# Performance work log

Hardware: AMD Instinct MI355X
Metric: run time of the kernel (lower is better)

The kernel has to match this reference:

```python
import jax, jax.numpy as jnp
import numpy as np

B, S, D = 2, 2048, 2048
H, HKV = 16, 4
HD = D // H  # 128
ROPE_BASE = 10000.0


def _rope(t, cos, sin):
    # t: [B, h, S, HD]; torch variant: x1 = even dims, x2 = odd dims,
    # output = concat([x1*cos - x2*sin, x1*sin + x2*cos], axis=-1)
    x1 = t[..., ::2]
    x2 = t[..., 1::2]
    return jnp.concatenate([x1 * cos - x2 * sin, x1 * sin + x2 * cos], axis=-1)


def setup_inputs() -> dict:
    key = jax.random.key(0)
    kx, kq, kk, kv, ko = jax.random.split(key, 5)
    x = jax.random.normal(kx, (B, S, D), dtype=jnp.float32)
    scale = 0.02
    Wq = jax.random.normal(kq, (D, H * HD), dtype=jnp.float32) * scale
    Wk = jax.random.normal(kk, (D, HKV * HD), dtype=jnp.float32) * scale
    Wv = jax.random.normal(kv, (D, HKV * HD), dtype=jnp.float32) * scale
    Wo = jax.random.normal(ko, (H * HD, D), dtype=jnp.float32) * scale
    mask = jnp.tril(jnp.ones((S, S), dtype=bool))  # causal
    return {"x": x, "Wq": Wq, "Wk": Wk, "Wv": Wv, "Wo": Wo, "mask": mask}


def reference(x, Wq, Wk, Wv, Wo, mask):
    b, s, d = x.shape
    # projections: [B,S,h,HD] -> [B,h,S,HD]
    q = (x @ Wq).reshape(b, s, H, HD).transpose(0, 2, 1, 3)
    k = (x @ Wk).reshape(b, s, HKV, HD).transpose(0, 2, 1, 3)
    v = (x @ Wv).reshape(b, s, HKV, HD).transpose(0, 2, 1, 3)

    # RoPE tables: [S, HD/2]
    theta = 1.0 / (ROPE_BASE ** (jnp.arange(0, HD, 2, dtype=jnp.float32) / HD))
    angles = jnp.arange(s, dtype=jnp.float32)[:, None] * theta
    cos, sin = jnp.cos(angles), jnp.sin(angles)

    q = _rope(q, cos, sin)
    k = _rope(k, cos, sin)

    # GQA: repeat_interleave kv heads along head dim
    rep = H // HKV
    k = jnp.repeat(k, rep, axis=1)
    v = jnp.repeat(v, rep, axis=1)

    scores = jnp.einsum("bhqd,bhkd->bhqk", q, k) / jnp.sqrt(jnp.float32(HD))
    scores = jnp.where(mask, scores, -jnp.inf)
    attn = jax.nn.softmax(scores, axis=-1)

    out = jnp.einsum("bhqk,bhkd->bqhd", attn, v).reshape(b, s, H * HD)
    return out @ Wo
```

## Files before the change

kernel.cpp:

```cpp
#include <hip/hip_runtime.h>

typedef __bf16 bf16;
typedef __bf16 bf16x8 __attribute__((ext_vector_type(8)));
typedef float f32x4 __attribute__((ext_vector_type(4)));
typedef short s16x4 __attribute__((ext_vector_type(4)));

#define B_ 2
#define S_ 2048
#define D_ 2048
#define H_ 16
#define HKV_ 4
#define HD_ 128
#define QKVW 3072
#define QKW 2560
#define SCALE 0.08838834764831845f
#define NEGINF -30000.0f

__device__ inline void gload16(const void* g, void* l) {
  __builtin_amdgcn_global_load_lds((const __attribute__((address_space(1))) unsigned int*)g,
                                   (__attribute__((address_space(3))) unsigned int*)l, 16, 0, 0);
}

__device__ inline unsigned short bfb(float v) {
  union { bf16 h; unsigned short u; } c;
  c.h = (bf16)v;
  return c.u;
}

__global__ void detect_dtype(const unsigned* __restrict__ xw, int* __restrict__ flag) {
  __shared__ int cnt;
  if (threadIdx.x == 0) cnt = 0;
  __syncthreads();
  unsigned w = xw[(size_t)threadIdx.x * 16384];
  unsigned low = w & 0xFFFFu;
  int e = (int)((low >> 7) & 0xFF);
  int vote = (low == 0u || (e >= 100 && e <= 140)) ? 1 : 0;
  atomicAdd(&cnt, vote);
  __syncthreads();
  if (threadIdx.x == 0) *flag = (cnt >= 128) ? 1 : 0;
}

__global__ __launch_bounds__(256) void transpose_qkvw(
    const void* __restrict__ Wq, const void* __restrict__ Wk, const void* __restrict__ Wv,
    bf16* __restrict__ wqkvT, const int* __restrict__ flag) {
  int z = blockIdx.z;
  const void* in = (z == 0) ? Wq : (z == 1) ? Wk : Wv;
  int cols = (z == 0) ? 2048 : 512;
  bf16* out = wqkvT + ((z == 0) ? 0 : (z == 1) ? 2048 * 2048 : 2560 * 2048);
  if (blockIdx.x * 32 >= cols) return;
  int fm = *flag;
  __shared__ float tile[32][33];
  int c0 = blockIdx.x * 32, r0 = blockIdx.y * 32;
  int tx = threadIdx.x, ty = threadIdx.y;
#pragma unroll
  for (int i = 0; i < 32; i += 8) {
    long idx = (long)(r0 + ty + i) * cols + c0 + tx;
    tile[ty + i][tx] = fm ? (float)((const bf16*)in)[idx] : ((const float*)in)[idx];
  }
  __syncthreads();
#pragma unroll
  for (int i = 0; i < 32; i += 8)
    out[(long)(c0 + ty + i) * 2048 + r0 + tx] = (bf16)tile[tx][ty + i];
}

__global__ __launch_bounds__(256) void transpose_cvt(
    const void* __restrict__ in, bf16* __restrict__ out,
    long in_stride, long out_stride, const int* __restrict__ flag) {
  __shared__ float tile[32][33];
  int fm = *flag;
  int c0 = blockIdx.x * 32, r0 = blockIdx.y * 32;
  int tx = threadIdx.x, ty = threadIdx.y;
#pragma unroll
  for (int i = 0; i < 32; i += 8) {
    long idx = (long)(r0 + ty + i) * in_stride + c0 + tx;
    tile[ty + i][tx] = fm ? (float)((const bf16*)in)[idx] : ((const float*)in)[idx];
  }
  __syncthreads();
#pragma unroll
  for (int i = 0; i < 32; i += 8)
    out[(long)(c0 + ty + i) * out_stride + r0 + tx] = (bf16)tile[tx][ty + i];
}

#define BM 128
#define BN 128
#define BK 32

__global__ __launch_bounds__(256) void gemm_bt(
    const void* __restrict__ A, const bf16* __restrict__ Bt, void* __restrict__ C,
    int M, int N, int K, int ldc, int ncmax,
    bf16* __restrict__ vt_out, int vcol0,
    const int* __restrict__ flag, int adyn, int cdyn) {
  alignas(16) __shared__ bf16 la[3 * BM * BK];
  alignas(16) __shared__ bf16 lb[3 * BN * BK];
  int fm = flag ? *flag : 1;
  bool af32 = adyn && !fm;
  bool cf32 = cdyn && !fm;
  int tid = threadIdx.x;
  int wave = tid >> 6, lane = tid & 63;
  int wr = wave >> 1, wc = wave & 1;
  int quad = lane >> 4, l16 = lane & 15;

  int nwg = (int)(gridDim.x * gridDim.y);
  int flat = (int)(blockIdx.y * gridDim.x + blockIdx.x);
  int cpx = nwg >> 3;
  int wk = (flat & 7) * cpx + (flat >> 3);
  int bx = wk % (int)gridDim.x, by = wk / (int)gridDim.x;
  int m0 = by * BM, n0 = bx * BN;

  f32x4 acc[4][4] = {};

  int sr = (wave << 4) + (lane >> 2);
  int sc = (lane & 3) << 3;
  const bf16* gb0 = Bt + (long)(n0 + sr) * K + sc;
  const bf16* gb1 = Bt + (long)(n0 + 64 + sr) * K + sc;
  int lo0 = (wave << 9);
  int lo1 = 2048 + (wave << 9);
  const bf16* ga0 = nullptr; const bf16* ga1 = nullptr;
  const float* gaf = nullptr;
  int fr = tid >> 1, fh = (tid & 1) << 4;
  if (af32) gaf = (const float*)A + (long)(m0 + fr) * K + fh;
  else { ga0 = (const bf16*)A + (long)(m0 + sr) * K + sc;
         ga1 = (const bf16*)A + (long)(m0 + 64 + sr) * K + sc; }
  int lawo = fr * BK + fh;

  int nk = K / BK;

  auto stageB = [&](int T, int buf) {
    int k0 = T * BK;
    bf16* d = lb + (buf << 12);
    gload16(gb0 + k0, d + lo0);
    gload16(gb1 + k0, d + lo1);
  };
  auto stageA = [&](int T, int buf) {
    int k0 = T * BK;
    bf16* d = la + (buf << 12);
    gload16(ga0 + k0, d + lo0);
    gload16(ga1 + k0, d + lo1);
  };
  auto loadA = [&](int T, float4* f) {
    const float* fp = gaf + (long)T * BK;
#pragma unroll
    for (int u = 0; u < 4; u++) f[u] = *(const float4*)(fp + 4 * u);
  };
  auto cvtwrite = [&](const float4* f, int buf) {
    alignas(16) bf16 tt[16];
#pragma unroll
    for (int u = 0; u < 4; u++) {
      tt[4 * u] = (bf16)f[u].x; tt[4 * u + 1] = (bf16)f[u].y;
      tt[4 * u + 2] = (bf16)f[u].z; tt[4 * u + 3] = (bf16)f[u].w;
    }
    bf16* d = la + (buf << 12) + lawo;
    *(uint4*)d = *(uint4*)tt;
    *(uint4*)(d + 8) = *(uint4*)(tt + 8);
  };
  auto compute = [&](int buf) {
    const bf16* pa = la + (buf << 12) + ((wr << 6) + l16) * BK + (quad << 3);
    const bf16* pb = lb + (buf << 12) + ((wc << 6) + l16) * BK + (quad << 3);
    bf16x8 afr[4], bfr[4];
#pragma unroll
    for (int i = 0; i < 4; i++) afr[i] = *(const bf16x8*)(pa + (i << 4) * BK);
#pragma unroll
    for (int j = 0; j < 4; j++) bfr[j] = *(const bf16x8*)(pb + (j << 4) * BK);
#pragma unroll
    for (int i = 0; i < 4; i++)
#pragma unroll
      for (int j = 0; j < 4; j++)
        acc[i][j] = __builtin_amdgcn_mfma_f32_16x16x32_bf16(afr[i], bfr[j], acc[i][j], 0, 0, 0);
  };

  if (!af32) {
    stageB(0, 0); stageA(0, 0);
    stageB(1, 1); stageA(1, 1);
    for (int t = 0; t + 2 < nk; ++t) {
      int bS = (t + 2) % 3, bC = t % 3;
      stageB(t + 2, bS);
      stageA(t + 2, bS);
      asm volatile("s_waitcnt vmcnt(8)" ::: "memory");
      __builtin_amdgcn_s_barrier();
      compute(bC);
      __builtin_amdgcn_s_barrier();
    }
    asm volatile("s_waitcnt vmcnt(4)" ::: "memory");
    __builtin_amdgcn_s_barrier();
    compute((nk - 2) % 3);
    asm volatile("s_waitcnt vmcnt(0)" ::: "memory");
    __builtin_amdgcn_s_barrier();
    compute((nk - 1) % 3);
  } else {
    float4 fP[4], fN[4];
    stageB(0, 0); loadA(0, fP); cvtwrite(fP, 0);
    stageB(1, 1); loadA(1, fP); cvtwrite(fP, 1);
    for (int t = 0; t + 2 < nk; ++t) {
      int bS = (t + 2) % 3, bC = t % 3;
      stageB(t + 2, bS);
      loadA(t + 2, fN);
      if (t > 0) cvtwrite(fP, (t + 1) % 3);
      asm volatile("s_waitcnt vmcnt(12) lgkmcnt(0)" ::: "memory");
      __builtin_amdgcn_s_barrier();
      compute(bC);
      __builtin_amdgcn_s_barrier();
#pragma unroll
      for (int u = 0; u < 4; u++) fP[u] = fN[u];
    }
    cvtwrite(fP, (nk - 1) % 3);
    compute((nk - 2) % 3);
    asm volatile("s_waitcnt vmcnt(0) lgkmcnt(0)" ::: "memory");
    __builtin_amdgcn_s_barrier();
    compute((nk - 1) % 3);
  }

  if (vt_out && n0 >= vcol0) {
#pragma unroll
    for (int i = 0; i < 4; i++)
#pragma unroll
      for (int j = 0; j < 4; j++) {
        int col = n0 + (wc << 6) + (j << 4) + l16;
        int hdg = col - vcol0;
        int row0 = m0 + (wr << 6) + (i << 4) + (quad << 2);
        int bb = row0 >> 11, s = row0 & 2047;
        ushort4 p;
        p.x = bfb(acc[i][j][0]); p.y = bfb(acc[i][j][1]);
        p.z = bfb(acc[i][j][2]); p.w = bfb(acc[i][j][3]);
        *(ushort4*)(vt_out + (((long)(bb * 512 + hdg)) << 11) + s) = p;
      }
  } else {
#pragma unroll
    for (int i = 0; i < 4; i++)
#pragma unroll
      for (int j = 0; j < 4; j++) {
        int col = n0 + (wc << 6) + (j << 4) + l16;
        if (col >= ncmax) continue;
#pragma unroll
        for (int r = 0; r < 4; r++) {
          long row = m0 + (wr << 6) + (i << 4) + (quad << 2) + r;
          float v = acc[i][j][r];
          if (cf32) ((float*)C)[row * ldc + col] = v;
          else      ((bf16*)C)[row * ldc + col] = (bf16)v;
        }
      }
  }
}

__global__ __launch_bounds__(256) void rope_scatter(
    const bf16* __restrict__ qkv, bf16* __restrict__ Q, bf16* __restrict__ Ko) {
  int row = blockIdx.x;
  int b = row >> 11, s = row & 2047;
  int tid = threadIdx.x;
  const bf16* src = qkv + (long)row * QKW;
#pragma unroll
  for (int it = 0; it < 4; ++it) {
    int p = tid + it * 256;
    int h = p >> 6, i = p & 63;
    float x1 = (float)src[h * 128 + 2 * i];
    float x2 = (float)src[h * 128 + 2 * i + 1];
    float theta = __expf(-0.14391156831212787f * (float)i);
    float sn, cs;
    sincosf((float)s * theta, &sn, &cs);
    long qb = ((long)(b * H_ + h) * S_ + s) * HD_;
    Q[qb + i]      = (bf16)((x1 * cs - x2 * sn) * SCALE);
    Q[qb + 64 + i] = (bf16)((x1 * sn + x2 * cs) * SCALE);
  }
  {
    int kh = tid >> 6, i = tid & 63;
    float x1 = (float)src[2048 + kh * 128 + 2 * i];
    float x2 = (float)src[2048 + kh * 128 + 2 * i + 1];
    float theta = __expf(-0.14391156831212787f * (float)i);
    float sn, cs;
    sincosf((float)s * theta, &sn, &cs);
    long kb = ((long)(b * HKV_ + kh) * S_ + s) * HD_;
    Ko[kb + i]      = (bf16)(x1 * cs - x2 * sn);
    Ko[kb + 64 + i] = (bf16)(x1 * sn + x2 * cs);
  }
}

#define KTILE 8192
#define VTILE 8192

__global__ __launch_bounds__(256) void attn_kernel(
    const bf16* __restrict__ Q, const bf16* __restrict__ K,
    const bf16* __restrict__ Vt, bf16* __restrict__ O) {
  alignas(16) __shared__ bf16 Ks[2 * KTILE];
  alignas(16) __shared__ bf16 Vs[2 * VTILE];
  int qt0 = blockIdx.x;
  int h = blockIdx.y, b = blockIdx.z;
  int kh = h >> 2;
  int tid = threadIdx.x, wave = tid >> 6, lane = tid & 63;
  int quad = lane >> 4, l16 = lane & 15;
  const bf16* Kg = K + ((long)(b * HKV_ + kh) * S_) * HD_;
  const bf16* Vg = Vt + ((long)(b * HKV_ + kh) * HD_) * S_;

  int kgo[4], vgo[4], klo[4], vlo[4];
#pragma unroll
  for (int u = 0; u < 4; u++) {
    int i = u * 4 + wave;
    int r = i * 4 + quad;
    int c = l16 ^ (r & 15);
    kgo[u] = r * HD_ + c * 8;
    klo[u] = i * 512;
    int v = i * 8 + (lane >> 3);
    int cv = (lane & 7) ^ (v & 7);
    vgo[u] = v * S_ + cv * 8;
    vlo[u] = i * 512;
  }

  for (int hf = 0; hf < 2; ++hf) {
    int qt = hf ? 31 - qt0 : qt0;
    int q0 = qt * 64;
    const bf16* Qg = Q + ((long)(b * H_ + h) * S_ + q0) * HD_;

    bf16x8 qb[4];
    {
      const bf16* qrow = Qg + (wave * 16 + l16) * HD_ + quad * 8;
#pragma unroll
      for (int kk = 0; kk < 4; kk++) qb[kk] = *(const bf16x8*)(qrow + kk * 32);
    }

    if (hf) __syncthreads();

#pragma unroll
    for (int u = 0; u < 4; u++) {
      gload16(Kg + kgo[u], Ks + klo[u]);
      gload16(Vg + vgo[u], Vs + vlo[u]);
    }

    f32x4 Of[8] = {};
    float m_run = NEGINF, l_run = 0.f;

    for (int kt = 0; kt <= qt; ++kt) {
      __syncthreads();
      int p = kt & 1;
      if (kt < qt) {
        const bf16* kn = Kg + (long)(kt + 1) * 8192;
        const bf16* vn = Vg + (long)(kt + 1) * 64;
        bf16* kd = Ks + (p ^ 1) * KTILE;
        bf16* vd = Vs + (p ^ 1) * VTILE;
#pragma unroll
        for (int u = 0; u < 4; u++) {
          gload16(kn + kgo[u], kd + klo[u]);
          gload16(vn + vgo[u], vd + vlo[u]);
        }
      }
      const bf16* kc = Ks + p * KTILE;
      const bf16* vc = Vs + p * VTILE;

      bool diag = (kt == qt);
      f32x4 sf[4];
      __builtin_amdgcn_s_setprio(1);
#pragma unroll
      for (int jb = 0; jb < 4; jb++) {
        if (diag && jb > wave) {
          sf[jb] = (f32x4){NEGINF, NEGINF, NEGINF, NEGINF};
        } else {
          f32x4 a = {};
          const bf16* kbase = kc + (jb * 16 + l16) * 128;
#pragma unroll
          for (int kk = 0; kk < 4; kk++) {
            bf16x8 kf = *(const bf16x8*)(kbase + (((kk * 4 + quad) ^ l16) * 8));
            a = __builtin_amdgcn_mfma_f32_16x16x32_bf16(kf, qb[kk], a, 0, 0, 0);
          }
          sf[jb] = a;
        }
      }
      __builtin_amdgcn_s_setprio(0);
      if (diag) {
#pragma unroll
        for (int jb = 0; jb < 4; jb++)
          if (jb == wave) {
#pragma unroll
            for (int r = 0; r < 4; r++)
              if (quad * 4 + r > l16) sf[jb][r] = NEGINF;
          }
      }

      float mx = NEGINF;
#pragma unroll
      for (int jb = 0; jb < 4; jb++)
#pragma unroll
        for (int r = 0; r < 4; r++) mx = fmaxf(mx, sf[jb][r]);
      mx = fmaxf(mx, __shfl_xor(mx, 16));
      mx = fmaxf(mx, __shfl_xor(mx, 32));
      if (__any(mx > m_run + 8.0f)) {
        float mnew = fmaxf(m_run, mx);
        float alpha = __expf(m_run - mnew);
        m_run = mnew;
        l_run *= alpha;
#pragma unroll
        for (int n = 0; n < 8; n++) Of[n] *= alpha;
      }

      float ls = 0.f;
      s16x4 pk[4];
#pragma unroll
      for (int jb = 0; jb < 4; jb++) {
        float p0 = __expf(sf[jb][0] - m_run);
        float p1 = __expf(sf[jb][1] - m_run);
        float p2 = __expf(sf[jb][2] - m_run);
        float p3 = __expf(sf[jb][3] - m_run);
        ls += (p0 + p1) + (p2 + p3);
        s16x4 t;
        t.x = (short)bfb(p0); t.y = (short)bfb(p1);
        t.z = (short)bfb(p2); t.w = (short)bfb(p3);
        pk[jb] = t;
      }
      l_run += ls;

      __builtin_amdgcn_s_setprio(1);
#pragma unroll
      for (int jb = 0; jb < 4; jb++) {
        if (diag && jb > wave) continue;
#pragma unroll
        for (int n = 0; n < 8; n++) {
          int v = n * 16 + l16;
          const bf16* va_p = vc + v * 64 + (((jb * 2 + (quad >> 1)) ^ (l16 & 7)) * 8) + (quad & 1) * 4;
          s16x4 va = *(const s16x4*)va_p;
          Of[n] = __builtin_amdgcn_mfma_f32_16x16x16bf16_1k(va, pk[jb], Of[n], 0, 0, 0);
        }
      }
      __builtin_amdgcn_s_setprio(0);
    }

    l_run += __shfl_xor(l_run, 16);
    l_run += __shfl_xor(l_run, 32);
    float inv = 1.0f / fmaxf(l_run, 1e-30f);
    bf16* Ob = O + ((long)(b * S_) + q0 + wave * 16 + l16) * D_ + h * HD_;
#pragma unroll
    for (int n = 0; n < 8; n++) {
      ushort4 w;
      w.x = bfb(Of[n][0] * inv); w.y = bfb(Of[n][1] * inv);
      w.z = bfb(Of[n][2] * inv); w.w = bfb(Of[n][3] * inv);
      *(ushort4*)(Ob + n * 16 + quad * 4) = w;
    }
  }
}

extern "C" void kernel_launch(void* const* d_in, const int* in_sizes, int n_in,
                              void* d_out, int out_size, void* d_ws, size_t ws_size,
                              hipStream_t stream) {
  const void* x  = d_in[0];
  const void* Wq = d_in[1];
  const void* Wk = d_in[2];
  const void* Wv = d_in[3];
  const void* Wo = d_in[4];
  bf16* ws = (bf16*)d_ws;
  int* flag = (int*)d_ws;

  bf16* qkv   = ws + 16;
  bf16* Vtb   = ws + 10485776;
  bf16* Qb    = ws + 12582928;
  bf16* wqkvT = ws + 12582928;
  bf16* Kb    = ws + 20971536;
  bf16* attno = ws + 16;
  bf16* woT   = ws + 10485776;

  dim3 tb(32, 8);
  detect_dtype<<<1, 256, 0, stream>>>((const unsigned*)x, flag);
  transpose_qkvw<<<dim3(64, 64, 3), tb, 0, stream>>>(Wq, Wk, Wv, wqkvT, flag);
  gemm_bt<<<dim3(QKVW / BN, (B_ * S_) / BM), 256, 0, stream>>>(
      x, wqkvT, qkv, B_ * S_, QKVW, D_, QKW, QKW, Vtb, QKW, flag, 1, 0);
  rope_scatter<<<B_ * S_, 256, 0, stream>>>(qkv, Qb, Kb);
  attn_kernel<<<dim3(S_ / 128, H_, B_), 256, 0, stream>>>(Qb, Kb, Vtb, attno);
  transpose_cvt<<<dim3(64, 64, 1), tb, 0, stream>>>(Wo, woT, 2048, 2048, flag);
  gemm_bt<<<dim3(D_ / BN, (B_ * S_) / BM), 256, 0, stream>>>(
      attno, woT, d_out, B_ * S_, D_, D_, D_, D_, nullptr, 0, flag, 0, 1);
}
```

Measured before the change: 440.1 us.

## Switch GEMM LDS pipeline from triple to double buffering

Reduces the GEMM shared-memory staging from three buffers to two and restructures the prefetch loop, with new wait counts and barriers placed around each compute step. Halving LDS use per block (from 48KB to 32KB) could allow more resident workgroups per CU and so improve latency hiding. In exchange, each tile has less prefetch lead time, and in the fp32-A path the convert-and-write of the next tile now runs after compute, which can expose load latency. Inline-asm memory fences are wrapped around the barriers.

```diff
diff --git a/kernel.cpp b/kernel.cpp
--- a/kernel.cpp
+++ b/kernel.cpp
@@ -25,6 +25,12 @@
   union { bf16 h; unsigned short u; } c;
   c.h = (bf16)v;
   return c.u;
+}
+
+__device__ inline void bar() {
+  asm volatile("" ::: "memory");
+  __builtin_amdgcn_s_barrier();
+  asm volatile("" ::: "memory");
 }
 
 __global__ void detect_dtype(const unsigned* __restrict__ xw, int* __restrict__ flag) {
@@ -90,8 +96,8 @@
     int M, int N, int K, int ldc, int ncmax,
     bf16* __restrict__ vt_out, int vcol0,
     const int* __restrict__ flag, int adyn, int cdyn) {
-  alignas(16) __shared__ bf16 la[3 * BM * BK];
-  alignas(16) __shared__ bf16 lb[3 * BN * BK];
+  alignas(16) __shared__ bf16 la[2 * BM * BK];
+  alignas(16) __shared__ bf16 lb[2 * BN * BK];
   int fm = flag ? *flag : 1;
   bool af32 = adyn && !fm;
   bool cf32 = cdyn && !fm;
@@ -170,43 +176,42 @@
 
   if (!af32) {
     stageB(0, 0); stageA(0, 0);
-    stageB(1, 1); stageA(1, 1);
-    for (int t = 0; t + 2 < nk; ++t) {
-      int bS = (t + 2) % 3, bC = t % 3;
-      stageB(t + 2, bS);
-      stageA(t + 2, bS);
-      asm volatile("s_waitcnt vmcnt(8)" ::: "memory");
-      __builtin_amdgcn_s_barrier();
-      compute(bC);
-      __builtin_amdgcn_s_barrier();
-    }
-    asm volatile("s_waitcnt vmcnt(4)" ::: "memory");
-    __builtin_amdgcn_s_barrier();
-    compute((nk - 2) % 3);
     asm volatile("s_waitcnt vmcnt(0)" ::: "memory");
-    __builtin_amdgcn_s_barrier();
-    compute((nk - 1) % 3);
+    bar();
+    for (int t = 0; t < nk - 1; ++t) {
+      stageB(t + 1, (t + 1) & 1);
+      stageA(t + 1, (t + 1) & 1);
+      asm volatile("s_waitcnt vmcnt(4)" ::: "memory");
+      bar();
+      compute(t & 1);
+      bar();
+    }
+    asm volatile("s_waitcnt vmcnt(0)" ::: "memory");
+    bar();
+    compute((nk - 1) & 1);
   } else {
-    float4 fP[4], fN[4];
-    stageB(0, 0); loadA(0, fP); cvtwrite(fP, 0);
-    stageB(1, 1); loadA(1, fP); cvtwrite(fP, 1);
-    for (int t = 0; t + 2 < nk; ++t) {
-      int bS = (t + 2) % 3, bC = t % 3;
-      stageB(t + 2, bS);
-      loadA(t + 2, fN);
-      if (t > 0) cvtwrite(fP, (t + 1) % 3);
-      asm volatile("s_waitcnt vmcnt(12) lgkmcnt(0)" ::: "memory");
-      __builtin_amdgcn_s_barrier();
-      compute(bC);
-      __builtin_amdgcn_s_barrier();
-#pragma unroll
-      for (int u = 0; u < 4; u++) fP[u] = fN[u];
-    }
-    cvtwrite(fP, (nk - 1) % 3);
-    compute((nk - 2) % 3);
-    asm volatile("s_waitcnt vmcnt(0) lgkmcnt(0)" ::: "memory");
-    __builtin_amdgcn_s_barrier();
-    compute((nk - 1) % 3);
+    stageB(0, 0);
+    { float4 f0[4]; loadA(0, f0); cvtwrite(f0, 0); }
+    float4 fP[4];
+    loadA(1, fP);
+    asm volatile("s_waitcnt lgkmcnt(0)" ::: "memory");
+    bar();
+    for (int t = 0; t < nk - 1; ++t) {
+      stageB(t + 1, (t + 1) & 1);
+      float4 fN[4];
+      bool hasF = (t + 2 < nk);
+      if (hasF) loadA(t + 2, fN);
+      asm volatile("s_waitcnt vmcnt(6)" ::: "memory");
+      bar();
+      compute(t & 1);
+      cvtwrite(fP, (t + 1) & 1);
+      if (hasF) { fP[0] = fN[0]; fP[1] = fN[1]; fP[2] = fN[2]; fP[3] = fN[3]; }
+      asm volatile("s_waitcnt lgkmcnt(0)" ::: "memory");
+      bar();
+    }
+    asm volatile("s_waitcnt vmcnt(0)" ::: "memory");
+    bar();
+    compute((nk - 1) & 1);
   }
 
   if (vt_out && n0 >= vcol0) {
```

Result: faster. 398.6 us (-9.4%).
